# Kernel tuning notes

Measured on AMD Instinct MI355X. Metric: run time of the kernel, lower is better.

Reference implementation:

```python
import jax, jax.numpy as jnp
import numpy as np

B, C, H, W = 16, 32, 256, 256


def _dir_scan(xT, w_seq):
    """Forward-direction linear recurrence with ReLU clamp.
    xT: (L, B, C, D) input moved so scanned axis is leading.
    w_seq: (L-1, D) per-step gates (broadcast over B, C).
    out[0] = xT[0]; out[i] = relu(w_seq[i-1] * out[i-1] + xT[i]).
    """
    def step(prev, xs):
        xr, wr = xs
        new = jnp.maximum(wr * prev + xr, 0.0)
        return new, new
    _, outs = jax.lax.scan(step, xT[0], (xT[1:], w_seq))
    return jnp.concatenate([xT[:1], outs], axis=0)


def _forward(inp, weights, conv_w, conv_b):
    w_up, w_down, w_left, w_right = jax.nn.sigmoid(weights)  # each (H, W)

    # scans along H: rows weighted by w[i] of shape (W,)
    xH = jnp.moveaxis(inp, 2, 0)  # (H, B, C, W)
    uc = jnp.moveaxis(_dir_scan(xH, w_up[:-1]), 0, 2)
    dc = jnp.moveaxis(_dir_scan(xH[::-1], w_down[::-1][:-1])[::-1], 0, 2)

    # scans along W: cols weighted by w[:, i] of shape (H,)
    xW = jnp.moveaxis(inp, 3, 0)  # (W, B, C, H)
    lc = jnp.moveaxis(_dir_scan(xW, w_left.T[:-1]), 0, 3)
    rc = jnp.moveaxis(_dir_scan(xW[::-1], w_right.T[::-1][:-1])[::-1], 0, 3)

    ctx = jnp.concatenate([lc, rc, uc, dc], axis=1)  # (B, 4C, H, W)
    out = jnp.einsum('bkhw,ck->bchw', ctx, conv_w) + conv_b[None, :, None, None]
    return jnp.maximum(out, 0.0)


def setup_inputs() -> dict:
    key = jax.random.key(0)
    k1, k2, k3, k4 = jax.random.split(key, 4)
    inp = jax.random.normal(k1, (B, C, H, W), dtype=jnp.float32)
    weights = jax.random.normal(k2, (4, H, W), dtype=jnp.float32) * 0.1
    conv_w = jax.random.normal(k3, (C, 4 * C), dtype=jnp.float32) / np.sqrt(4 * C)
    conv_b = jax.random.normal(k4, (C,), dtype=jnp.float32) * 0.01
    return {"inp": inp, "weights": weights, "conv_w": conv_w, "conv_b": conv_b}


def reference(inp, weights, conv_w, conv_b):
    return _forward(inp, weights, conv_w, conv_b)
```

## Files before the change

### kernel.cpp

```cpp
#include <hip/hip_runtime.h>
#include <hip/hip_fp16.h>

#define B_ 16
#define C_ 32
#define H_ 256
#define W_ 256
#define HW_ (H_*W_)
#define NPIX ((size_t)B_*C_*HW_)

static const size_t WS_SIG = 0;
static const size_t WS_WT  = (size_t)1 << 20;
static const size_t WS_UC  = ((size_t)1 << 20) + (64u << 10);
static const size_t WS_DC  = WS_UC + NPIX * 2;
static const size_t WS_NEED = WS_DC + NPIX * 2;

#define SWZIDX(c, w) (((c) << 8) | ((w) ^ (((c) & 7) << 2) ^ (((w) >> 6) & 3)))
#define GSW(w) ((w) ^ ((((w) >> 5) & 7) << 2))

__global__ __launch_bounds__(256) void k_sigmoid(const float* __restrict__ w,
                                                 float* __restrict__ sw) {
    int i = blockIdx.x * 256 + threadIdx.x;
    float x = w[i];
    sw[i] = 1.0f / (1.0f + expf(-x));
}

__global__ __launch_bounds__(256) void k_wT(const float* __restrict__ cw,
                                            float* __restrict__ wT) {
    int i = blockIdx.x * 256 + threadIdx.x;
    int k = i >> 5, c = i & 31;
    wT[i] = cw[c * 128 + k];
}

__global__ __launch_bounds__(256) void k_vscan(const float* __restrict__ inp,
                                               const float* __restrict__ sw,
                                               __half* __restrict__ uc,
                                               __half* __restrict__ dc) {
    int blk = blockIdx.x, t = threadIdx.x, bc = blk & 511;
    const float* xb = inp + (size_t)bc * HW_ + t;
    if (blk < 512) {
        const float* gb = sw + t;
        __half* ob = uc + (size_t)bc * HW_ + t;
        float cur = xb[0];
        ob[0] = __float2half(cur);
        float p0 = xb[1*W_], p1 = xb[2*W_], p2 = xb[3*W_], p3 = xb[4*W_];
        float q0 = gb[0*W_], q1 = gb[1*W_], q2 = gb[2*W_], q3 = gb[3*W_];
        #pragma unroll 1
        for (int h = 1; h <= 245; h += 4) {
            float n0 = xb[(h+4)*W_], n1 = xb[(h+5)*W_];
            float n2 = xb[(h+6)*W_], n3 = xb[(h+7)*W_];
            float m0 = gb[(h+3)*W_], m1 = gb[(h+4)*W_];
            float m2 = gb[(h+5)*W_], m3 = gb[(h+6)*W_];
            cur = fmaxf(fmaf(q0, cur, p0), 0.f); ob[(h+0)*W_] = __float2half(cur);
            cur = fmaxf(fmaf(q1, cur, p1), 0.f); ob[(h+1)*W_] = __float2half(cur);
            cur = fmaxf(fmaf(q2, cur, p2), 0.f); ob[(h+2)*W_] = __float2half(cur);
            cur = fmaxf(fmaf(q3, cur, p3), 0.f); ob[(h+3)*W_] = __float2half(cur);
            p0 = n0; p1 = n1; p2 = n2; p3 = n3;
            q0 = m0; q1 = m1; q2 = m2; q3 = m3;
        }
        cur = fmaxf(fmaf(q0, cur, p0), 0.f); ob[249*W_] = __float2half(cur);
        cur = fmaxf(fmaf(q1, cur, p1), 0.f); ob[250*W_] = __float2half(cur);
        cur = fmaxf(fmaf(q2, cur, p2), 0.f); ob[251*W_] = __float2half(cur);
        cur = fmaxf(fmaf(q3, cur, p3), 0.f); ob[252*W_] = __float2half(cur);
        for (int h = 253; h < 256; ++h) {
            cur = fmaxf(fmaf(gb[(h-1)*W_], cur, xb[h*W_]), 0.f);
            ob[h*W_] = __float2half(cur);
        }
    } else {
        const float* gb = sw + HW_ + t;
        __half* ob = dc + (size_t)bc * HW_ + t;
        float cur = xb[255*W_];
        ob[255*W_] = __float2half(cur);
        float p0 = xb[254*W_], p1 = xb[253*W_], p2 = xb[252*W_], p3 = xb[251*W_];
        float q0 = gb[255*W_], q1 = gb[254*W_], q2 = gb[253*W_], q3 = gb[252*W_];
        #pragma unroll 1
        for (int r = 254; r >= 10; r -= 4) {
            float n0 = xb[(r-4)*W_], n1 = xb[(r-5)*W_];
            float n2 = xb[(r-6)*W_], n3 = xb[(r-7)*W_];
            float m0 = gb[(r-3)*W_], m1 = gb[(r-4)*W_];
            float m2 = gb[(r-5)*W_], m3 = gb[(r-6)*W_];
            cur = fmaxf(fmaf(q0, cur, p0), 0.f); ob[(r-0)*W_] = __float2half(cur);
            cur = fmaxf(fmaf(q1, cur, p1), 0.f); ob[(r-1)*W_] = __float2half(cur);
            cur = fmaxf(fmaf(q2, cur, p2), 0.f); ob[(r-2)*W_] = __float2half(cur);
            cur = fmaxf(fmaf(q3, cur, p3), 0.f); ob[(r-3)*W_] = __float2half(cur);
            p0 = n0; p1 = n1; p2 = n2; p3 = n3;
            q0 = m0; q1 = m1; q2 = m2; q3 = m3;
        }
        cur = fmaxf(fmaf(q0, cur, p0), 0.f); ob[6*W_] = __float2half(cur);
        cur = fmaxf(fmaf(q1, cur, p1), 0.f); ob[5*W_] = __float2half(cur);
        cur = fmaxf(fmaf(q2, cur, p2), 0.f); ob[4*W_] = __float2half(cur);
        cur = fmaxf(fmaf(q3, cur, p3), 0.f); ob[3*W_] = __float2half(cur);
        for (int r = 2; r >= 0; --r) {
            cur = fmaxf(fmaf(gb[(r+1)*W_], cur, xb[r*W_]), 0.f);
            ob[r*W_] = __float2half(cur);
        }
    }
}

__global__ __launch_bounds__(256) void k_hconv(const float* __restrict__ inp,
                                               const float* __restrict__ sw,
                                               const float* __restrict__ wT,
                                               const float* __restrict__ bias,
                                               const __half* __restrict__ uc,
                                               const __half* __restrict__ dc,
                                               float* __restrict__ out) {
    __shared__ float  sx[C_ * W_];
    __shared__ __half src[C_ * W_];
    __shared__ float  sgl[W_];
    __shared__ float  sgr[W_];
    int bid = blockIdx.x;
    int b = bid >> 8;
    int h = bid & 255;
    int t = threadIdx.x;
    int lane = t & 63;
    int tm = (t >> 6) & 3;

    const float* ibase = inp + (size_t)b * C_ * HW_ + (size_t)h * W_;
    #pragma unroll 8
    for (int c = 0; c < C_; ++c)
        sx[SWZIDX(c, t)] = ibase[(size_t)c * HW_ + t];
    sgl[GSW(t)] = sw[2 * HW_ + h * W_ + t];
    sgr[GSW(t)] = sw[3 * HW_ + h * W_ + t];
    __syncthreads();

    int c = t >> 3, s = t & 7;
    int cbase = c << 8;
    int cm = (c & 7) << 2;
    int sm = (s >> 1) & 3;
    int ws = s << 5;

    float x0   = sx[cbase | (0 ^ cm)];
    float x255 = sx[cbase | (255 ^ cm ^ 3)];

    float lA, lB, lC;
    {
        int w0 = (s == 0) ? 1 : ws;
        lA = sgl[GSW(w0 - 1)];
        lB = sx[cbase | (w0 ^ cm ^ sm)];
        lC = 0.f;
        for (int w = w0 + 1; w <= ws + 31; ++w) {
            float g  = sgl[GSW(w - 1)];
            float xv = sx[cbase | (w ^ cm ^ sm)];
            lA = g * lA;
            lB = fmaf(g, lB, xv);
            lC = fmaxf(fmaf(g, lC, xv), 0.f);
        }
    }
    float rA, rB, rC;
    {
        int w1 = (s == 7) ? 254 : (ws + 31);
        rA = sgr[GSW(w1 + 1)];
        rB = sx[cbase | (w1 ^ cm ^ sm)];
        rC = 0.f;
        for (int w = w1 - 1; w >= ws; --w) {
            float g  = sgr[GSW(w + 1)];
            float xv = sx[cbase | (w ^ cm ^ sm)];
            rA = g * rA;
            rB = fmaf(g, rB, xv);
            rC = fmaxf(fmaf(g, rC, xv), 0.f);
        }
    }

    #pragma unroll
    for (int off = 1; off < 8; off <<= 1) {
        int sl = (s >= off) ? (lane - off) : lane;
        float pA = __shfl(lA, sl), pB = __shfl(lB, sl), pC = __shfl(lC, sl);
        float nA = lA * pA;
        float nB = fmaf(lA, pB, lB);
        float nC = fmaxf(fmaf(lA, pC, lB), lC);
        if (s >= off) { lA = nA; lB = nB; lC = nC; }
        int sr = (s + off <= 7) ? (lane + off) : lane;
        float qA = __shfl(rA, sr), qB = __shfl(rB, sr), qC = __shfl(rC, sr);
        float mA = rA * qA;
        float mB = fmaf(rA, qB, rB);
        float mC = fmaxf(fmaf(rA, qC, rB), rC);
        if (s + off <= 7) { rA = mA; rB = mB; rC = mC; }
    }
    int slm = (s >= 1) ? (lane - 1) : lane;
    float aA = __shfl(lA, slm), aB = __shfl(lB, slm), aC = __shfl(lC, slm);
    float lv = (s == 0) ? x0 : fmaxf(fmaf(aA, x0, aB), aC);
    int srp = (s <= 6) ? (lane + 1) : lane;
    float bA = __shfl(rA, srp), bB = __shfl(rB, srp), bC = __shfl(rC, srp);
    float rv = (s == 7) ? x255 : fmaxf(fmaf(bA, x255, bB), bC);

    {
        float v = rv;
        if (s == 7) src[cbase | (255 ^ cm ^ 3)] = __float2half(x255);
        int wend = (s == 7) ? 254 : (ws + 31);
        for (int w = wend; w >= ws; --w) {
            float xv = sx[cbase | (w ^ cm ^ sm)];
            v = fmaxf(fmaf(sgr[GSW(w + 1)], v, xv), 0.f);
            src[cbase | (w ^ cm ^ sm)] = __float2half(v);
        }
    }
    {
        float v = lv;
        int wst = (s == 0) ? 1 : ws;
        for (int w = wst; w <= ws + 31; ++w) {
            float xv = sx[cbase | (w ^ cm ^ sm)];
            v = fmaxf(fmaf(sgl[GSW(w - 1)], v, xv), 0.f);
            sx[cbase | (w ^ cm ^ sm)] = v;
        }
    }
    __syncthreads();

    float acc[C_];
    #pragma unroll
    for (int cc = 0; cc < C_; ++cc) acc[cc] = bias[cc];

    const __half* ucp = uc + (size_t)b * C_ * HW_ + (size_t)h * W_ + t;
    const __half* dcp = dc + (size_t)b * C_ * HW_ + (size_t)h * W_ + t;

    for (int cc = 0; cc < C_; ++cc) {
        int idx = (cc << 8) | (t ^ ((cc & 7) << 2) ^ tm);
        float vl = sx[idx];
        float vr = __half2float(src[idx]);
        float vu = __half2float(ucp[(size_t)cc * HW_]);
        float vd = __half2float(dcp[(size_t)cc * HW_]);
        const float* w0 = wT + cc * C_;
        const float* w1 = wT + (32 + cc) * C_;
        const float* w2 = wT + (64 + cc) * C_;
        const float* w3 = wT + (96 + cc) * C_;
        #pragma unroll
        for (int k = 0; k < C_; ++k) {
            float a = acc[k];
            a = fmaf(w0[k], vl, a);
            a = fmaf(w1[k], vr, a);
            a = fmaf(w2[k], vu, a);
            a = fmaf(w3[k], vd, a);
            acc[k] = a;
        }
    }

    float* obase = out + (size_t)b * C_ * HW_ + (size_t)h * W_ + t;
    #pragma unroll
    for (int k = 0; k < C_; ++k) {
        obase[(size_t)k * HW_] = fmaxf(acc[k], 0.0f);
    }
}

extern "C" void kernel_launch(void* const* d_in, const int* in_sizes, int n_in,
                              void* d_out, int out_size, void* d_ws, size_t ws_size,
                              hipStream_t stream) {
    const float* inp     = (const float*)d_in[0];
    const float* weights = (const float*)d_in[1];
    const float* conv_w  = (const float*)d_in[2];
    const float* conv_b  = (const float*)d_in[3];
    float* out = (float*)d_out;

    if (ws_size < WS_NEED) return;

    char* ws = (char*)d_ws;
    float*  sw  = (float*)(ws + WS_SIG);
    float*  wT  = (float*)(ws + WS_WT);
    __half* uc  = (__half*)(ws + WS_UC);
    __half* dc  = (__half*)(ws + WS_DC);

    k_sigmoid<<<1024, 256, 0, stream>>>(weights, sw);
    k_wT<<<16, 256, 0, stream>>>(conv_w, wT);
    k_vscan<<<1024, 256, 0, stream>>>(inp, sw, uc, dc);
    k_hconv<<<B_ * H_, 256, 0, stream>>>(inp, sw, wT, conv_b, uc, dc, out);
}
```

Before: 455.6 us.

## Use packed fp16 dot2 for channel mix and halve LDS footprint in hconv

The horizontal-scan/conv kernel now stores the input row and the left/right scan results as interleaved fp16 pairs in LDS, which halves shared memory from about 48KB to 32KB so more blocks can be resident (launch bounds ask for 4 per CU). The 1x1 channel mix packs conv weights as fp16 pairs and uses v_dot2 (fdot2) with fp32 accumulation, halving the FMA instruction count. The vertical scan kernel is unrolled 8-deep with deeper prefetch, and its blocks are interleaved so up and down directions for the same channels run together. Holding the left context and the input in fp16 reduces precision relative to the previous fp32 path.

```diff
diff --git a/kernel.cpp b/kernel.cpp
--- a/kernel.cpp
+++ b/kernel.cpp
@@ -14,54 +14,75 @@
 static const size_t WS_DC  = WS_UC + NPIX * 2;
 static const size_t WS_NEED = WS_DC + NPIX * 2;
 
-#define SWZIDX(c, w) (((c) << 8) | ((w) ^ (((c) & 7) << 2) ^ (((w) >> 6) & 3)))
+typedef _Float16 v2h __attribute__((ext_vector_type(2)));
+
+#if defined(__has_builtin)
+# if __has_builtin(__builtin_amdgcn_fdot2)
+#  define HAVE_FDOT2 1
+# endif
+#endif
+
+static __device__ __forceinline__ v2h as_v2h(unsigned int u) {
+    union { unsigned int i; v2h h; } x; x.i = u; return x.h;
+}
+
+#define PIDX(c, w) (((c) << 8) | ((w) ^ (((c) & 7) << 2) ^ (((w) >> 6) & 3)))
 #define GSW(w) ((w) ^ ((((w) >> 5) & 7) << 2))
 
 __global__ __launch_bounds__(256) void k_sigmoid(const float* __restrict__ w,
                                                  float* __restrict__ sw) {
     int i = blockIdx.x * 256 + threadIdx.x;
-    float x = w[i];
-    sw[i] = 1.0f / (1.0f + expf(-x));
-}
-
-__global__ __launch_bounds__(256) void k_wT(const float* __restrict__ cw,
-                                            float* __restrict__ wT) {
+    sw[i] = 1.0f / (1.0f + expf(-w[i]));
+}
+
+__global__ __launch_bounds__(256) void k_pack(const float* __restrict__ cw,
+                                              unsigned int* __restrict__ pw) {
     int i = blockIdx.x * 256 + threadIdx.x;
-    int k = i >> 5, c = i & 31;
-    wT[i] = cw[c * 128 + k];
+    int p = i >> 10, cc = (i >> 5) & 31, k = i & 31;
+    int base = k * 128 + (p ? 64 : 0) + cc;
+    __half lo = __float2half(cw[base]);
+    __half hi = __float2half(cw[base + 32]);
+    pw[i] = (unsigned int)(*(unsigned short*)&lo) |
+            ((unsigned int)(*(unsigned short*)&hi) << 16);
 }
 
 __global__ __launch_bounds__(256) void k_vscan(const float* __restrict__ inp,
                                                const float* __restrict__ sw,
                                                __half* __restrict__ uc,
                                                __half* __restrict__ dc) {
-    int blk = blockIdx.x, t = threadIdx.x, bc = blk & 511;
+    int blk = blockIdx.x, t = threadIdx.x;
+    int g = blk >> 4, r = blk & 15;
+    int dir = r >> 3;
+    int bc = g * 8 + (r & 7);
     const float* xb = inp + (size_t)bc * HW_ + t;
-    if (blk < 512) {
+    float p[8], q[8], np[8], nq[8];
+    if (dir == 0) {
         const float* gb = sw + t;
         __half* ob = uc + (size_t)bc * HW_ + t;
         float cur = xb[0];
         ob[0] = __float2half(cur);
-        float p0 = xb[1*W_], p1 = xb[2*W_], p2 = xb[3*W_], p3 = xb[4*W_];
-        float q0 = gb[0*W_], q1 = gb[1*W_], q2 = gb[2*W_], q3 = gb[3*W_];
+        #pragma unroll
+        for (int j = 0; j < 8; ++j) { p[j] = xb[(1+j)*W_]; q[j] = gb[j*W_]; }
         #pragma unroll 1
-        for (int h = 1; h <= 245; h += 4) {
-            float n0 = xb[(h+4)*W_], n1 = xb[(h+5)*W_];
-            float n2 = xb[(h+6)*W_], n3 = xb[(h+7)*W_];
-            float m0 = gb[(h+3)*W_], m1 = gb[(h+4)*W_];
-            float m2 = gb[(h+5)*W_], m3 = gb[(h+6)*W_];
-            cur = fmaxf(fmaf(q0, cur, p0), 0.f); ob[(h+0)*W_] = __float2half(cur);
-            cur = fmaxf(fmaf(q1, cur, p1), 0.f); ob[(h+1)*W_] = __float2half(cur);
-            cur = fmaxf(fmaf(q2, cur, p2), 0.f); ob[(h+2)*W_] = __float2half(cur);
-            cur = fmaxf(fmaf(q3, cur, p3), 0.f); ob[(h+3)*W_] = __float2half(cur);
-            p0 = n0; p1 = n1; p2 = n2; p3 = n3;
-            q0 = m0; q1 = m1; q2 = m2; q3 = m3;
-        }
-        cur = fmaxf(fmaf(q0, cur, p0), 0.f); ob[249*W_] = __float2half(cur);
-        cur = fmaxf(fmaf(q1, cur, p1), 0.f); ob[250*W_] = __float2half(cur);
-        cur = fmaxf(fmaf(q2, cur, p2), 0.f); ob[251*W_] = __float2half(cur);
-        cur = fmaxf(fmaf(q3, cur, p3), 0.f); ob[252*W_] = __float2half(cur);
-        for (int h = 253; h < 256; ++h) {
+        for (int h0 = 1; h0 <= 233; h0 += 8) {
+            #pragma unroll
+            for (int j = 0; j < 8; ++j) {
+                np[j] = xb[(h0+8+j)*W_]; nq[j] = gb[(h0+7+j)*W_];
+            }
+            #pragma unroll
+            for (int j = 0; j < 8; ++j) {
+                cur = fmaxf(fmaf(q[j], cur, p[j]), 0.f);
+                ob[(h0+j)*W_] = __float2half(cur);
+            }
+            #pragma unroll
+            for (int j = 0; j < 8; ++j) { p[j] = np[j]; q[j] = nq[j]; }
+        }
+        #pragma unroll
+        for (int j = 0; j < 8; ++j) {
+            cur = fmaxf(fmaf(q[j], cur, p[j]), 0.f);
+            ob[(241+j)*W_] = __float2half(cur);
+        }
+        for (int h = 249; h < 256; ++h) {
             cur = fmaxf(fmaf(gb[(h-1)*W_], cur, xb[h*W_]), 0.f);
             ob[h*W_] = __float2half(cur);
         }
@@ -70,54 +91,55 @@
         __half* ob = dc + (size_t)bc * HW_ + t;
         float cur = xb[255*W_];
         ob[255*W_] = __float2half(cur);
-        float p0 = xb[254*W_], p1 = xb[253*W_], p2 = xb[252*W_], p3 = xb[251*W_];
-        float q0 = gb[255*W_], q1 = gb[254*W_], q2 = gb[253*W_], q3 = gb[252*W_];
+        #pragma unroll
+        for (int j = 0; j < 8; ++j) { p[j] = xb[(254-j)*W_]; q[j] = gb[(255-j)*W_]; }
         #pragma unroll 1
-        for (int r = 254; r >= 10; r -= 4) {
-            float n0 = xb[(r-4)*W_], n1 = xb[(r-5)*W_];
-            float n2 = xb[(r-6)*W_], n3 = xb[(r-7)*W_];
-            float m0 = gb[(r-3)*W_], m1 = gb[(r-4)*W_];
-            float m2 = gb[(r-5)*W_], m3 = gb[(r-6)*W_];
-            cur = fmaxf(fmaf(q0, cur, p0), 0.f); ob[(r-0)*W_] = __float2half(cur);
-            cur = fmaxf(fmaf(q1, cur, p1), 0.f); ob[(r-1)*W_] = __float2half(cur);
-            cur = fmaxf(fmaf(q2, cur, p2), 0.f); ob[(r-2)*W_] = __float2half(cur);
-            cur = fmaxf(fmaf(q3, cur, p3), 0.f); ob[(r-3)*W_] = __float2half(cur);
-            p0 = n0; p1 = n1; p2 = n2; p3 = n3;
-            q0 = m0; q1 = m1; q2 = m2; q3 = m3;
-        }
-        cur = fmaxf(fmaf(q0, cur, p0), 0.f); ob[6*W_] = __float2half(cur);
-        cur = fmaxf(fmaf(q1, cur, p1), 0.f); ob[5*W_] = __float2half(cur);
-        cur = fmaxf(fmaf(q2, cur, p2), 0.f); ob[4*W_] = __float2half(cur);
-        cur = fmaxf(fmaf(q3, cur, p3), 0.f); ob[3*W_] = __float2half(cur);
-        for (int r = 2; r >= 0; --r) {
-            cur = fmaxf(fmaf(gb[(r+1)*W_], cur, xb[r*W_]), 0.f);
-            ob[r*W_] = __float2half(cur);
-        }
-    }
-}
-
-__global__ __launch_bounds__(256) void k_hconv(const float* __restrict__ inp,
-                                               const float* __restrict__ sw,
-                                               const float* __restrict__ wT,
-                                               const float* __restrict__ bias,
-                                               const __half* __restrict__ uc,
-                                               const __half* __restrict__ dc,
-                                               float* __restrict__ out) {
-    __shared__ float  sx[C_ * W_];
-    __shared__ __half src[C_ * W_];
-    __shared__ float  sgl[W_];
-    __shared__ float  sgr[W_];
+        for (int r0 = 254; r0 >= 22; r0 -= 8) {
+            #pragma unroll
+            for (int j = 0; j < 8; ++j) {
+                np[j] = xb[(r0-8-j)*W_]; nq[j] = gb[(r0-7-j)*W_];
+            }
+            #pragma unroll
+            for (int j = 0; j < 8; ++j) {
+                cur = fmaxf(fmaf(q[j], cur, p[j]), 0.f);
+                ob[(r0-j)*W_] = __float2half(cur);
+            }
+            #pragma unroll
+            for (int j = 0; j < 8; ++j) { p[j] = np[j]; q[j] = nq[j]; }
+        }
+        #pragma unroll
+        for (int j = 0; j < 8; ++j) {
+            cur = fmaxf(fmaf(q[j], cur, p[j]), 0.f);
+            ob[(14-j)*W_] = __float2half(cur);
+        }
+        for (int rr = 6; rr >= 0; --rr) {
+            cur = fmaxf(fmaf(gb[(rr+1)*W_], cur, xb[rr*W_]), 0.f);
+            ob[rr*W_] = __float2half(cur);
+        }
+    }
+}
+
+__global__ __launch_bounds__(256, 4) void k_hconv(const float* __restrict__ inp,
+                                                  const float* __restrict__ sw,
+                                                  const unsigned int* __restrict__ pw,
+                                                  const float* __restrict__ bias,
+                                                  const __half* __restrict__ uc,
+                                                  const __half* __restrict__ dc,
+                                                  float* __restrict__ out) {
+    __shared__ unsigned int spair[C_ * W_];
+    __shared__ float sgl[W_];
+    __shared__ float sgr[W_];
+    __half* hp = (__half*)spair;
     int bid = blockIdx.x;
     int b = bid >> 8;
     int h = bid & 255;
     int t = threadIdx.x;
     int lane = t & 63;
-    int tm = (t >> 6) & 3;
 
     const float* ibase = inp + (size_t)b * C_ * HW_ + (size_t)h * W_;
     #pragma unroll 8
     for (int c = 0; c < C_; ++c)
-        sx[SWZIDX(c, t)] = ibase[(size_t)c * HW_ + t];
+        hp[2 * PIDX(c, t)] = __float2half(ibase[(size_t)c * HW_ + t]);
     sgl[GSW(t)] = sw[2 * HW_ + h * W_ + t];
     sgr[GSW(t)] = sw[3 * HW_ + h * W_ + t];
     __syncthreads();
@@ -128,35 +150,35 @@
     int sm = (s >> 1) & 3;
     int ws = s << 5;
 
-    float x0   = sx[cbase | (0 ^ cm)];
-    float x255 = sx[cbase | (255 ^ cm ^ 3)];
+    float x0   = __half2float(hp[2 * (cbase | (0 ^ cm))]);
+    float x255 = __half2float(hp[2 * (cbase | (255 ^ cm ^ 3))]);
 
     float lA, lB, lC;
     {
         int w0 = (s == 0) ? 1 : ws;
         lA = sgl[GSW(w0 - 1)];
-        lB = sx[cbase | (w0 ^ cm ^ sm)];
+        lB = __half2float(hp[2 * (cbase | (w0 ^ cm ^ sm))]);
         lC = 0.f;
         for (int w = w0 + 1; w <= ws + 31; ++w) {
-            float g  = sgl[GSW(w - 1)];
-            float xv = sx[cbase | (w ^ cm ^ sm)];
-            lA = g * lA;
-            lB = fmaf(g, lB, xv);
-            lC = fmaxf(fmaf(g, lC, xv), 0.f);
+            float gv = sgl[GSW(w - 1)];
+            float xv = __half2float(hp[2 * (cbase | (w ^ cm ^ sm))]);
+            lA = gv * lA;
+            lB = fmaf(gv, lB, xv);
+            lC = fmaxf(fmaf(gv, lC, xv), 0.f);
         }
     }
     float rA, rB, rC;
     {
         int w1 = (s == 7) ? 254 : (ws + 31);
         rA = sgr[GSW(w1 + 1)];
-        rB = sx[cbase | (w1 ^ cm ^ sm)];
+        rB = __half2float(hp[2 * (cbase | (w1 ^ cm ^ sm))]);
         rC = 0.f;
         for (int w = w1 - 1; w >= ws; --w) {
-            float g  = sgr[GSW(w + 1)];
-            float xv = sx[cbase | (w ^ cm ^ sm)];
-            rA = g * rA;
-            rB = fmaf(g, rB, xv);
-            rC = fmaxf(fmaf(g, rC, xv), 0.f);
+            float gv = sgr[GSW(w + 1)];
+            float xv = __half2float(hp[2 * (cbase | (w ^ cm ^ sm))]);
+            rA = gv * rA;
+            rB = fmaf(gv, rB, xv);
+            rC = fmaxf(fmaf(gv, rC, xv), 0.f);
         }
     }
 
@@ -184,54 +206,70 @@
 
     {
         float v = rv;
-        if (s == 7) src[cbase | (255 ^ cm ^ 3)] = __float2half(x255);
+        if (s == 7) hp[2 * (cbase | (255 ^ cm ^ 3)) + 1] = __float2half(x255);
         int wend = (s == 7) ? 254 : (ws + 31);
         for (int w = wend; w >= ws; --w) {
-            float xv = sx[cbase | (w ^ cm ^ sm)];
+            int idx = cbase | (w ^ cm ^ sm);
+            float xv = __half2float(hp[2 * idx]);
             v = fmaxf(fmaf(sgr[GSW(w + 1)], v, xv), 0.f);
-            src[cbase | (w ^ cm ^ sm)] = __float2half(v);
+            hp[2 * idx + 1] = __float2half(v);
         }
     }
     {
         float v = lv;
         int wst = (s == 0) ? 1 : ws;
         for (int w = wst; w <= ws + 31; ++w) {
-            float xv = sx[cbase | (w ^ cm ^ sm)];
+            int idx = cbase | (w ^ cm ^ sm);
+            float xv = __half2float(hp[2 * idx]);
             v = fmaxf(fmaf(sgl[GSW(w - 1)], v, xv), 0.f);
-            sx[cbase | (w ^ cm ^ sm)] = v;
+            hp[2 * idx] = __float2half(v);
         }
     }
     __syncthreads();
 
     float acc[C_];
     #pragma unroll
-    for (int cc = 0; cc < C_; ++cc) acc[cc] = bias[cc];
-
-    const __half* ucp = uc + (size_t)b * C_ * HW_ + (size_t)h * W_ + t;
-    const __half* dcp = dc + (size_t)b * C_ * HW_ + (size_t)h * W_ + t;
-
+    for (int k = 0; k < C_; ++k) acc[k] = bias[k];
+
+    size_t pixbase = (size_t)b * C_ * HW_ + (size_t)h * W_ + t;
+    const unsigned short* ucp = (const unsigned short*)uc + pixbase;
+    const unsigned short* dcp = (const unsigned short*)dc + pixbase;
+    int tm = (t >> 6) & 3;
+
+    #pragma unroll 4
     for (int cc = 0; cc < C_; ++cc) {
-        int idx = (cc << 8) | (t ^ ((cc & 7) << 2) ^ tm);
-        float vl = sx[idx];
-        float vr = __half2float(src[idx]);
-        float vu = __half2float(ucp[(size_t)cc * HW_]);
-        float vd = __half2float(dcp[(size_t)cc * HW_]);
-        const float* w0 = wT + cc * C_;
-        const float* w1 = wT + (32 + cc) * C_;
-        const float* w2 = wT + (64 + cc) * C_;
-        const float* w3 = wT + (96 + cc) * C_;
+        unsigned int lr = spair[(cc << 8) | (t ^ ((cc & 7) << 2) ^ tm)];
+        unsigned int u = ucp[(size_t)cc * HW_];
+        unsigned int d = dcp[(size_t)cc * HW_];
+        unsigned int ud = u | (d << 16);
+        v2h vlr = as_v2h(lr);
+        v2h vud = as_v2h(ud);
+        const unsigned int* w1 = pw + cc * 32;
+        const unsigned int* w2 = pw + 1024 + cc * 32;
+#ifdef HAVE_FDOT2
         #pragma unroll
         for (int k = 0; k < C_; ++k) {
-            float a = acc[k];
-            a = fmaf(w0[k], vl, a);
-            a = fmaf(w1[k], vr, a);
-            a = fmaf(w2[k], vu, a);
-            a = fmaf(w3[k], vd, a);
-            acc[k] = a;
-        }
-    }
-
-    float* obase = out + (size_t)b * C_ * HW_ + (size_t)h * W_ + t;
+            acc[k] = __builtin_amdgcn_fdot2(vlr, as_v2h(w1[k]), acc[k], false);
+            acc[k] = __builtin_amdgcn_fdot2(vud, as_v2h(w2[k]), acc[k], false);
+        }
+#else
+        float vl = (float)vlr.x, vr = (float)vlr.y;
+        float vu = (float)vud.x, vd = (float)vud.y;
+        #pragma unroll
+        for (int k = 0; k < C_; ++k) {
+            v2h a = as_v2h(w1[k]);
+            v2h bb = as_v2h(w2[k]);
+            float av = acc[k];
+            av = fmaf((float)a.x, vl, av);
+            av = fmaf((float)a.y, vr, av);
+            av = fmaf((float)bb.x, vu, av);
+            av = fmaf((float)bb.y, vd, av);
+            acc[k] = av;
+        }
+#endif
+    }
+
+    float* obase = out + pixbase;
     #pragma unroll
     for (int k = 0; k < C_; ++k) {
         obase[(size_t)k * HW_] = fmaxf(acc[k], 0.0f);
@@ -250,13 +288,13 @@
     if (ws_size < WS_NEED) return;
 
     char* ws = (char*)d_ws;
-    float*  sw  = (float*)(ws + WS_SIG);
-    float*  wT  = (float*)(ws + WS_WT);
-    __half* uc  = (__half*)(ws + WS_UC);
-    __half* dc  = (__half*)(ws + WS_DC);
+    float*        sw = (float*)(ws + WS_SIG);
+    unsigned int* pw = (unsigned int*)(ws + WS_WT);
+    __half*       uc = (__half*)(ws + WS_UC);
+    __half*       dc = (__half*)(ws + WS_DC);
 
     k_sigmoid<<<1024, 256, 0, stream>>>(weights, sw);
-    k_wT<<<16, 256, 0, stream>>>(conv_w, wT);
+    k_pack<<<8, 256, 0, stream>>>(conv_w, pw);
     k_vscan<<<1024, 256, 0, stream>>>(inp, sw, uc, dc);
-    k_hconv<<<B_ * H_, 256, 0, stream>>>(inp, sw, wT, conv_b, uc, dc, out);
-}
+    k_hconv<<<B_ * H_, 256, 0, stream>>>(inp, sw, pw, conv_b, uc, dc, out);
+}
```

New measurement: 405.5 us. 1.12x faster.
